# Optimization experiments

Hardware: AMD Instinct MI355X
Metric: run time of the kernel (lower is better)

## Reference

```python
import jax, jax.numpy as jnp
import numpy as np

N, D = 8192, 64


def setup_inputs() -> dict:
    key = jax.random.key(0)
    X = jax.random.normal(key, (N, D), dtype=jnp.float32)
    return {"X": X}


def reference(X):
    # Pairwise Euclidean distance matrix d_X[i, j] = ||X[i] - X[j]||_2.
    # Same math as sqrt(sum((X[:,None,:] - X[None,:,:])**2, -1)) but computed
    # via the Gram-matrix identity to avoid the [N, N, D] intermediate.
    sq_norms = jnp.sum(X * X, axis=1)                      # [N]
    gram = jnp.einsum('id,jd->ij', X, X)                   # [N, N]
    sq = sq_norms[:, None] + sq_norms[None, :] - 2.0 * gram
    sq = jnp.maximum(sq, 0.0)                              # clamp fp round-off
    # safe sqrt: exact zeros (diagonal) stay 0 with finite grad
    pos = sq > 0.0
    d_X = jnp.where(pos, jnp.sqrt(jnp.where(pos, sq, 1.0)), 0.0)
    return d_X
```

## Files before the change

kernel.cpp:

```cpp
#include <hip/hip_runtime.h>

#define NN 8192
#define DD 64

typedef short bf16x8 __attribute__((ext_vector_type(8)));
typedef float f32x4 __attribute__((ext_vector_type(4)));

__device__ __forceinline__ unsigned short f2bf(float f) {
    unsigned int u = __float_as_uint(f);
    unsigned int r = (u + 0x7FFFu + ((u >> 16) & 1u)) >> 16;
    return (unsigned short)r;
}

__device__ __forceinline__ float fsqrt(float x) {
#if __has_builtin(__builtin_amdgcn_sqrtf)
    return __builtin_amdgcn_sqrtf(x);
#else
    return sqrtf(x);
#endif
}

__global__ __launch_bounds__(256) void rips_setup(const float* __restrict__ X,
                                                  unsigned short* __restrict__ Xb,
                                                  float* __restrict__ norms) {
    const int t   = blockIdx.x * 256 + threadIdx.x;
    const int row = t >> 3;
    const int j   = t & 7;
    const float* p = X + (size_t)row * DD + j * 8;
    float4 lo = *(const float4*)p;
    float4 hi = *(const float4*)(p + 4);

    bf16x8 v;
    v[0] = (short)f2bf(lo.x); v[1] = (short)f2bf(lo.y);
    v[2] = (short)f2bf(lo.z); v[3] = (short)f2bf(lo.w);
    v[4] = (short)f2bf(hi.x); v[5] = (short)f2bf(hi.y);
    v[6] = (short)f2bf(hi.z); v[7] = (short)f2bf(hi.w);
    *(bf16x8*)(Xb + (size_t)row * DD + j * 8) = v;

    float acc = lo.x*lo.x + lo.y*lo.y + lo.z*lo.z + lo.w*lo.w
              + hi.x*hi.x + hi.y*hi.y + hi.z*hi.z + hi.w*hi.w;
    acc += __shfl_xor(acc, 1);
    acc += __shfl_xor(acc, 2);
    acc += __shfl_xor(acc, 4);
    if (j == 0) norms[row] = acc;
}

__global__ __launch_bounds__(256) void rips_main(const unsigned short* __restrict__ Xb,
                                                 const float* __restrict__ norms,
                                                 float* __restrict__ out) {
    const int bid = blockIdx.x;
    const int rowBase = (bid >> 6) * 128;
    const int colBase = (bid & 63) * 128;

    const int tid  = threadIdx.x;
    const int lane = tid & 63;
    const int w    = tid >> 6;
    const int wr   = w >> 1;
    const int wc   = w & 1;

    __shared__ float rn[128];
    __shared__ float cn[128];
    __shared__ float stage[4][16 * 72];

    if (tid < 128) rn[tid]       = norms[rowBase + tid];
    else           cn[tid - 128] = norms[colBase + tid - 128];
    __syncthreads();

    const int fr = lane & 15;
    const int kg = lane >> 4;

    f32x4 acc[4][4];
    #pragma unroll
    for (int m = 0; m < 4; ++m)
        #pragma unroll
        for (int n = 0; n < 4; ++n)
            acc[m][n] = (f32x4){0.f, 0.f, 0.f, 0.f};

    #pragma unroll
    for (int kk = 0; kk < DD; kk += 32) {
        bf16x8 a[4], bfr[4];
        #pragma unroll
        for (int n = 0; n < 4; ++n)
            a[n] = *(const bf16x8*)(Xb + (size_t)(colBase + wc * 64 + n * 16 + fr) * DD + kk + kg * 8);
        #pragma unroll
        for (int m = 0; m < 4; ++m)
            bfr[m] = *(const bf16x8*)(Xb + (size_t)(rowBase + wr * 64 + m * 16 + fr) * DD + kk + kg * 8);
        #pragma unroll
        for (int m = 0; m < 4; ++m)
            #pragma unroll
            for (int n = 0; n < 4; ++n)
                acc[m][n] = __builtin_amdgcn_mfma_f32_16x16x32_bf16(a[n], bfr[m], acc[m][n], 0, 0, 0);
    }

    float* st = stage[w];
    const int lr = lane >> 4;
    const int lc = lane & 15;

    #pragma unroll
    for (int m = 0; m < 4; ++m) {
        const int row_l = wr * 64 + m * 16 + fr;
        const int grow  = rowBase + row_l;
        const float rnv = rn[row_l];
        #pragma unroll
        for (int n = 0; n < 4; ++n) {
            const int col0_l = wc * 64 + n * 16 + kg * 4;
            const int gcol0  = colBase + col0_l;
            const float4 cnv = *(const float4*)&cn[col0_l];
            f32x4 o;
            o[0] = fsqrt(fmaxf(rnv + cnv.x - 2.0f * acc[m][n][0], 0.0f));
            o[1] = fsqrt(fmaxf(rnv + cnv.y - 2.0f * acc[m][n][1], 0.0f));
            o[2] = fsqrt(fmaxf(rnv + cnv.z - 2.0f * acc[m][n][2], 0.0f));
            o[3] = fsqrt(fmaxf(rnv + cnv.w - 2.0f * acc[m][n][3], 0.0f));
            if (grow == gcol0 + 0) o[0] = 0.0f;
            if (grow == gcol0 + 1) o[1] = 0.0f;
            if (grow == gcol0 + 2) o[2] = 0.0f;
            if (grow == gcol0 + 3) o[3] = 0.0f;
            *(f32x4*)&st[fr * 72 + n * 16 + kg * 4] = o;
        }
        #pragma unroll
        for (int t = 0; t < 4; ++t) {
            const int R = t * 4 + lr;
            f32x4 v = *(const f32x4*)&st[R * 72 + lc * 4];
            const int srow = rowBase + wr * 64 + m * 16 + R;
            const int scol = colBase + wc * 64 + lc * 4;
            *(f32x4*)(out + (size_t)srow * NN + scol) = v;
        }
    }
}

__global__ __launch_bounds__(256) void rips_fallback(const float* __restrict__ X,
                                                     float* __restrict__ out) {
    const int rowBase = blockIdx.y * 128;
    const int colBase = blockIdx.x * 128;
    const int tid  = threadIdx.x;
    const int lane = tid & 63;
    const int w    = tid >> 6;
    const int wr   = w >> 1;
    const int wc   = w & 1;

    __shared__ float rn[128];
    __shared__ float cn[128];
    {
        const int idx  = tid & 127;
        const int base = (tid < 128) ? rowBase : colBase;
        const float4* p = (const float4*)(X + (size_t)(base + idx) * DD);
        float acc = 0.0f;
        #pragma unroll
        for (int i = 0; i < 16; ++i) {
            float4 v = p[i];
            acc += v.x * v.x + v.y * v.y + v.z * v.z + v.w * v.w;
        }
        if (tid < 128) rn[idx] = acc;
        else           cn[idx] = acc;
    }
    __syncthreads();

    f32x4 acc[4][4];
    #pragma unroll
    for (int m = 0; m < 4; ++m)
        #pragma unroll
        for (int n = 0; n < 4; ++n)
            acc[m][n] = (f32x4){0.f, 0.f, 0.f, 0.f};

    const int fr = lane & 15;
    const int kg = lane >> 4;

    #pragma unroll
    for (int kk = 0; kk < DD; kk += 32) {
        bf16x8 a[4], b[4];
        #pragma unroll
        for (int m = 0; m < 4; ++m) {
            const float* p = X + (size_t)(rowBase + wr * 64 + m * 16 + fr) * DD + kk + kg * 8;
            float4 lo = *(const float4*)p;
            float4 hi = *(const float4*)(p + 4);
            bf16x8 t;
            t[0] = (short)f2bf(lo.x); t[1] = (short)f2bf(lo.y);
            t[2] = (short)f2bf(lo.z); t[3] = (short)f2bf(lo.w);
            t[4] = (short)f2bf(hi.x); t[5] = (short)f2bf(hi.y);
            t[6] = (short)f2bf(hi.z); t[7] = (short)f2bf(hi.w);
            a[m] = t;
        }
        #pragma unroll
        for (int n = 0; n < 4; ++n) {
            const float* p = X + (size_t)(colBase + wc * 64 + n * 16 + fr) * DD + kk + kg * 8;
            float4 lo = *(const float4*)p;
            float4 hi = *(const float4*)(p + 4);
            bf16x8 t;
            t[0] = (short)f2bf(lo.x); t[1] = (short)f2bf(lo.y);
            t[2] = (short)f2bf(lo.z); t[3] = (short)f2bf(lo.w);
            t[4] = (short)f2bf(hi.x); t[5] = (short)f2bf(hi.y);
            t[6] = (short)f2bf(hi.z); t[7] = (short)f2bf(hi.w);
            b[n] = t;
        }
        #pragma unroll
        for (int m = 0; m < 4; ++m)
            #pragma unroll
            for (int n = 0; n < 4; ++n)
                acc[m][n] = __builtin_amdgcn_mfma_f32_16x16x32_bf16(a[m], b[n], acc[m][n], 0, 0, 0);
    }

    #pragma unroll
    for (int m = 0; m < 4; ++m) {
        #pragma unroll
        for (int n = 0; n < 4; ++n) {
            #pragma unroll
            for (int r = 0; r < 4; ++r) {
                const int row_l = wr * 64 + m * 16 + kg * 4 + r;
                const int col_l = wc * 64 + n * 16 + fr;
                const float g  = acc[m][n][r];
                float sq = rn[row_l] + cn[col_l] - 2.0f * g;
                sq = fmaxf(sq, 0.0f);
                float dv = sqrtf(sq);
                const int grow = rowBase + row_l;
                const int gcol = colBase + col_l;
                if (grow == gcol) dv = 0.0f;
                out[(size_t)grow * NN + gcol] = dv;
            }
        }
    }
}

extern "C" void kernel_launch(void* const* d_in, const int* in_sizes, int n_in,
                              void* d_out, int out_size, void* d_ws, size_t ws_size,
                              hipStream_t stream) {
    const float* X = (const float*)d_in[0];
    float* out = (float*)d_out;

    const size_t xb_bytes   = (size_t)NN * DD * sizeof(unsigned short);
    const size_t norm_bytes = (size_t)NN * sizeof(float);

    if (ws_size >= xb_bytes + norm_bytes) {
        unsigned short* Xb = (unsigned short*)d_ws;
        float* norms = (float*)((char*)d_ws + xb_bytes);
        rips_setup<<<dim3(NN * 8 / 256, 1, 1), dim3(256, 1, 1), 0, stream>>>(X, Xb, norms);
        rips_main<<<dim3(4096, 1, 1), dim3(256, 1, 1), 0, stream>>>(Xb, norms, out);
    } else {
        dim3 grid(NN / 128, NN / 128, 1);
        rips_fallback<<<grid, dim3(256, 1, 1), 0, stream>>>(X, out);
    }
}
```

Before: 56.71 us.

## Reshape output tiles to 32x512 with full-row warps and skip off-diagonal checks

New measurement: 65.19 us. +15.0%, slower.

```diff
diff --git a/kernel.cpp b/kernel.cpp
--- a/kernel.cpp
+++ b/kernel.cpp
@@ -49,80 +49,82 @@
                                                  const float* __restrict__ norms,
                                                  float* __restrict__ out) {
     const int bid = blockIdx.x;
-    const int rowBase = (bid >> 6) * 128;
-    const int colBase = (bid & 63) * 128;
+    const int rowBase = (bid >> 4) * 32;
+    const int colBase = (bid & 15) * 512;
 
     const int tid  = threadIdx.x;
     const int lane = tid & 63;
-    const int w    = tid >> 6;
-    const int wr   = w >> 1;
-    const int wc   = w & 1;
-
-    __shared__ float rn[128];
-    __shared__ float cn[128];
-    __shared__ float stage[4][16 * 72];
-
-    if (tid < 128) rn[tid]       = norms[rowBase + tid];
-    else           cn[tid - 128] = norms[colBase + tid - 128];
+    const int wc   = tid >> 6;
+
+    __shared__ float rn[32];
+    __shared__ float cn[512];
+    __shared__ float stage[4][16 * 132];
+
+    if (tid < 32) rn[tid] = norms[rowBase + tid];
+    cn[tid]       = norms[colBase + tid];
+    cn[tid + 256] = norms[colBase + tid + 256];
     __syncthreads();
 
     const int fr = lane & 15;
     const int kg = lane >> 4;
 
-    f32x4 acc[4][4];
-    #pragma unroll
-    for (int m = 0; m < 4; ++m)
-        #pragma unroll
-        for (int n = 0; n < 4; ++n)
+    const bool tileHasDiag = (rowBase >= colBase) && (rowBase < colBase + 512);
+
+    f32x4 acc[2][8];
+    #pragma unroll
+    for (int m = 0; m < 2; ++m)
+        #pragma unroll
+        for (int n = 0; n < 8; ++n)
             acc[m][n] = (f32x4){0.f, 0.f, 0.f, 0.f};
 
     #pragma unroll
     for (int kk = 0; kk < DD; kk += 32) {
-        bf16x8 a[4], bfr[4];
-        #pragma unroll
-        for (int n = 0; n < 4; ++n)
-            a[n] = *(const bf16x8*)(Xb + (size_t)(colBase + wc * 64 + n * 16 + fr) * DD + kk + kg * 8);
-        #pragma unroll
-        for (int m = 0; m < 4; ++m)
-            bfr[m] = *(const bf16x8*)(Xb + (size_t)(rowBase + wr * 64 + m * 16 + fr) * DD + kk + kg * 8);
-        #pragma unroll
-        for (int m = 0; m < 4; ++m)
+        bf16x8 a[8], b[2];
+        #pragma unroll
+        for (int n = 0; n < 8; ++n)
+            a[n] = *(const bf16x8*)(Xb + (size_t)(colBase + wc * 128 + n * 16 + fr) * DD + kk + kg * 8);
+        #pragma unroll
+        for (int m = 0; m < 2; ++m)
+            b[m] = *(const bf16x8*)(Xb + (size_t)(rowBase + m * 16 + fr) * DD + kk + kg * 8);
+        #pragma unroll
+        for (int m = 0; m < 2; ++m)
             #pragma unroll
-            for (int n = 0; n < 4; ++n)
-                acc[m][n] = __builtin_amdgcn_mfma_f32_16x16x32_bf16(a[n], bfr[m], acc[m][n], 0, 0, 0);
-    }
-
-    float* st = stage[w];
-    const int lr = lane >> 4;
-    const int lc = lane & 15;
-
-    #pragma unroll
-    for (int m = 0; m < 4; ++m) {
-        const int row_l = wr * 64 + m * 16 + fr;
-        const int grow  = rowBase + row_l;
-        const float rnv = rn[row_l];
-        #pragma unroll
-        for (int n = 0; n < 4; ++n) {
-            const int col0_l = wc * 64 + n * 16 + kg * 4;
-            const int gcol0  = colBase + col0_l;
-            const float4 cnv = *(const float4*)&cn[col0_l];
+            for (int n = 0; n < 8; ++n)
+                acc[m][n] = __builtin_amdgcn_mfma_f32_16x16x32_bf16(a[n], b[m], acc[m][n], 0, 0, 0);
+    }
+
+    float* st = stage[wc];
+    const int sr = lane >> 5;
+    const int sc = lane & 31;
+
+    #pragma unroll
+    for (int m = 0; m < 2; ++m) {
+        const int grow  = rowBase + m * 16 + fr;
+        const float rnv = rn[m * 16 + fr];
+        #pragma unroll
+        for (int n = 0; n < 8; ++n) {
+            const int col_l = wc * 128 + n * 16 + kg * 4;
+            const int gcol0 = colBase + col_l;
+            const float4 cnv = *(const float4*)&cn[col_l];
             f32x4 o;
             o[0] = fsqrt(fmaxf(rnv + cnv.x - 2.0f * acc[m][n][0], 0.0f));
             o[1] = fsqrt(fmaxf(rnv + cnv.y - 2.0f * acc[m][n][1], 0.0f));
             o[2] = fsqrt(fmaxf(rnv + cnv.z - 2.0f * acc[m][n][2], 0.0f));
             o[3] = fsqrt(fmaxf(rnv + cnv.w - 2.0f * acc[m][n][3], 0.0f));
-            if (grow == gcol0 + 0) o[0] = 0.0f;
-            if (grow == gcol0 + 1) o[1] = 0.0f;
-            if (grow == gcol0 + 2) o[2] = 0.0f;
-            if (grow == gcol0 + 3) o[3] = 0.0f;
-            *(f32x4*)&st[fr * 72 + n * 16 + kg * 4] = o;
-        }
-        #pragma unroll
-        for (int t = 0; t < 4; ++t) {
-            const int R = t * 4 + lr;
-            f32x4 v = *(const f32x4*)&st[R * 72 + lc * 4];
-            const int srow = rowBase + wr * 64 + m * 16 + R;
-            const int scol = colBase + wc * 64 + lc * 4;
+            if (tileHasDiag) {
+                if (grow == gcol0 + 0) o[0] = 0.0f;
+                if (grow == gcol0 + 1) o[1] = 0.0f;
+                if (grow == gcol0 + 2) o[2] = 0.0f;
+                if (grow == gcol0 + 3) o[3] = 0.0f;
+            }
+            *(f32x4*)&st[fr * 132 + n * 16 + kg * 4] = o;
+        }
+        #pragma unroll
+        for (int t = 0; t < 8; ++t) {
+            const int R = t * 2 + sr;
+            f32x4 v = *(const f32x4*)&st[R * 132 + sc * 4];
+            const int srow = rowBase + m * 16 + R;
+            const int scol = colBase + wc * 128 + sc * 4;
             *(f32x4*)(out + (size_t)srow * NN + scol) = v;
         }
     }
@@ -233,7 +235,7 @@
         unsigned short* Xb = (unsigned short*)d_ws;
         float* norms = (float*)((char*)d_ws + xb_bytes);
         rips_setup<<<dim3(NN * 8 / 256, 1, 1), dim3(256, 1, 1), 0, stream>>>(X, Xb, norms);
-        rips_main<<<dim3(4096, 1, 1), dim3(256, 1, 1), 0, stream>>>(Xb, norms, out);
+        rips_main<<<dim3((NN / 32) * (NN / 512), 1, 1), dim3(256, 1, 1), 0, stream>>>(Xb, norms, out);
     } else {
         dim3 grid(NN / 128, NN / 128, 1);
         rips_fallback<<<grid, dim3(256, 1, 1), 0, stream>>>(X, out);
```
